# Kernel tuning notes

Hardware: AMD Instinct MI355X
Metric: run time of the kernel (lower is better)

## Reference

```python
import jax, jax.numpy as jnp
import numpy as np

B, G, M, N, RBF, H = 8, 1024, 8, 2048, 50, 128
CUT_LO, CUT_HI = 0.0, 5.0
F = RBF * M * M  # 3200 = in_features of the basis projections


def setup_inputs() -> dict:
    key = jax.random.key(0)
    ks = jax.random.split(key, 8)
    x = jax.random.normal(ks[0], (B, N, 3), dtype=jnp.float32)
    # mapping: linear mixing of fine particles into G groups of M coarse particles
    W_map = jax.random.normal(ks[1], (G, M, N), dtype=jnp.float32) / np.float32(np.sqrt(N))
    W_left = jax.random.normal(ks[2], (H, F), dtype=jnp.float32) / np.float32(np.sqrt(F))
    W_right = jax.random.normal(ks[3], (H, F), dtype=jnp.float32) / np.float32(np.sqrt(F))
    fc1_w = jax.random.normal(ks[4], (H, H), dtype=jnp.float32) / np.float32(np.sqrt(H))
    fc1_b = jax.random.normal(ks[5], (H,), dtype=jnp.float32) * 0.01
    fc2_w = jax.random.normal(ks[6], (1, H), dtype=jnp.float32) / np.float32(np.sqrt(H))
    fc2_b = jax.random.normal(ks[7], (1,), dtype=jnp.float32) * 0.01
    return {"x": x, "W_map": W_map, "W_left": W_left, "W_right": W_right,
            "fc1_w": fc1_w, "fc1_b": fc1_b, "fc2_w": fc2_w, "fc2_b": fc2_b}


def reference(x, W_map, W_left, W_right, fc1_w, fc1_b, fc2_w, fc2_b):
    # ExpNormalSmearing constants (torchmd-net defaults, non-trainable)
    alpha = np.float32(5.0 / (CUT_HI - CUT_LO))
    means = jnp.linspace(np.float32(np.exp(-CUT_HI + CUT_LO)), 1.0, RBF, dtype=jnp.float32)
    beta = np.float32((2.0 / RBF * (1.0 - np.exp(-CUT_HI + CUT_LO))) ** -2)

    # mapping: [B,N,3] -> coarse grained [B,G,M,3]
    xc = jnp.einsum('gmn,bnd->bgmd', W_map, x)
    # pairwise deltas within each group: [B,G,M,M,3]
    delta = xc[:, :, None, :, :] - xc[:, :, :, None, :]
    dn = jnp.sqrt(jnp.sum(delta ** 2, axis=-1, keepdims=True) + 1e-5)  # [B,G,M,M,1]
    # cosine cutoff * exp-normal RBF -> [B,G,M,M,RBF]
    cutoff = 0.5 * (jnp.cos(dn * jnp.pi / CUT_HI) + 1.0) * (dn < CUT_HI)
    sm = cutoff * jnp.exp(-beta * (jnp.exp(alpha * (CUT_LO - dn)) - means) ** 2)
    sm = sm / (dn + 1e-5) ** 2
    # outer-product basis: [B,G,M,M,RBF,3] -> [B,G,F,3]
    basis = (delta[..., None, :] * sm[..., None]).reshape(B, G, F, 3)
    # dual projections over the F axis (Linear applied on swapped axes)
    left = jnp.einsum('hf,bgfd->bghd', W_left, basis)   # [B,G,H,3]
    right = jnp.einsum('hf,bgfd->bghd', W_right, basis)  # [B,G,H,3]
    att = jnp.sum(left * right, axis=-1) + 1e-5          # [B,G,H]
    att = jax.nn.logsumexp(att, axis=-2)                  # pool over groups -> [B,H]
    h = jax.nn.silu(att @ fc1_w.T + fc1_b)
    return h @ fc2_w.T + fc2_b  # [B,1]
```

## Files before the change

kernel.cpp:

```cpp
#include <hip/hip_runtime.h>
#include <hip/hip_bf16.h>
#include <math.h>

#define B_   8
#define G_   1024
#define M_   8
#define N_   2048
#define RBF_ 50
#define H_   128
#define PP_  28
#define RPP  64
#define KSTEPS (PP_*RPP/32)
#define TPB  32

#define OFF_A    0
#define SZ_A     (KSTEPS*16*64*8/2)
#define OFF_XC   (OFF_A + SZ_A)
#define SZ_XC    (B_*G_*M_*3)
#define OFF_ATT  (OFF_XC + SZ_XC)
#define SZ_ATT   (B_*H_*G_)
#define OFF_PART (OFF_ATT + SZ_ATT)
#define SZ_PART  (B_*32*H_*2)

#define M0_   0.006737946999085467f
#define STEP_ 0.020270858224508f
#define BETA_ 633.5087862829640f
#define C2_   25.68448448181152f
#define C3_   0.26031300425529f
#define BC_   0.59416621404589f

typedef __attribute__((ext_vector_type(8))) short s8v;
typedef __attribute__((ext_vector_type(4))) float f4v;

#define LBAR() do { \
    asm volatile("s_waitcnt lgkmcnt(0)\n\ts_barrier" ::: "memory"); \
    __builtin_amdgcn_sched_barrier(0); \
} while (0)

__device__ const int c_pi[28] = {0,0,0,0,0,0,0,1,1,1,1,1,1,2,2,2,2,2,3,3,3,3,4,4,4,5,5,6};
__device__ const int c_pj[28] = {1,2,3,4,5,6,7,2,3,4,5,6,7,3,4,5,6,7,4,5,6,7,5,6,7,6,7,7};

__device__ __forceinline__ unsigned short f2bf(float f) {
    unsigned int b = __float_as_uint(f);
    return (unsigned short)((b + 0x7FFFu + ((b >> 16) & 1u)) >> 16);
}

__global__ __launch_bounds__(256) void k_folda(const float* __restrict__ Wl,
                                               const float* __restrict__ Wr,
                                               float* __restrict__ ws) {
    int t = blockIdx.x * 256 + threadIdx.x;
    int lane = t & 63;
    int mt = (t >> 6) & 15;
    int kstep = t >> 10;
    int pp = kstep >> 1;
    int row = mt * 16 + (lane & 15);
    int side = row >> 7, h = row & 127;
    int r0 = (kstep & 1) * 32 + (lane >> 4) * 8;
    int i = c_pi[pp], j = c_pj[pp];
    const float* src = side ? Wr : Wl;
    const float* pij = src + h * 3200 + (i * 8 + j) * 50;
    const float* pji = src + h * 3200 + (j * 8 + i) * 50;
    s8v v;
#pragma unroll
    for (int e = 0; e < 8; ++e) {
        int r = r0 + e;
        float f = (r < 50) ? (pij[r] - pji[r]) : 0.f;
        v[e] = (short)f2bf(f);
    }
    ((s8v*)(ws + OFF_A))[t] = v;
}

__global__ __launch_bounds__(256, 2) void k_xc(const float* __restrict__ x,
                                               const float* __restrict__ Wm,
                                               float* __restrict__ ws) {
    __shared__ float4 x_s[6][256];
    __shared__ float  red[4][24][68];
    float* xc = ws + OFF_XC;

    int tid = threadIdx.x;
    int wave = tid >> 6, lane = tid & 63;
    int rowbase = blockIdx.x * 16 + wave * 4;

    f4v acc[4][6];
#pragma unroll
    for (int r = 0; r < 4; ++r)
#pragma unroll
        for (int p = 0; p < 6; ++p) acc[r][p] = (f4v)0.f;

#pragma unroll
    for (int p = 0; p < 6; ++p) {
        int bd0 = p * 4;
        float4 v;
        v.x = x[(bd0/3)*6144     + tid*3 + (bd0%3)];
        v.y = x[((bd0+1)/3)*6144 + tid*3 + ((bd0+1)%3)];
        v.z = x[((bd0+2)/3)*6144 + tid*3 + ((bd0+2)%3)];
        v.w = x[((bd0+3)/3)*6144 + tid*3 + ((bd0+3)%3)];
        x_s[p][tid] = v;
    }
    LBAR();

#pragma unroll 1
    for (int nc = 0; nc < 8; ++nc) {
        int n0 = nc * 256;
        float4 pf[6];
        if (nc < 7) {
            int n1 = n0 + 256;
#pragma unroll
            for (int p = 0; p < 6; ++p) {
                int bd0 = p * 4;
                pf[p].x = x[(bd0/3)*6144     + (n1+tid)*3 + (bd0%3)];
                pf[p].y = x[((bd0+1)/3)*6144 + (n1+tid)*3 + ((bd0+1)%3)];
                pf[p].z = x[((bd0+2)/3)*6144 + (n1+tid)*3 + ((bd0+2)%3)];
                pf[p].w = x[((bd0+3)/3)*6144 + (n1+tid)*3 + ((bd0+3)%3)];
            }
        }
        float wv[4][4];
#pragma unroll
        for (int r = 0; r < 4; ++r) {
            const float* wrow = Wm + (size_t)(rowbase + r) * 2048 + n0 + lane;
#pragma unroll
            for (int k = 0; k < 4; ++k) wv[r][k] = wrow[k * 64];
        }
#pragma unroll
        for (int k = 0; k < 4; ++k) {
            int nn = k * 64 + lane;
#pragma unroll
            for (int p = 0; p < 6; ++p) {
                float4 xq = x_s[p][nn];
#pragma unroll
                for (int r = 0; r < 4; ++r) {
                    acc[r][p].x += wv[r][k] * xq.x;
                    acc[r][p].y += wv[r][k] * xq.y;
                    acc[r][p].z += wv[r][k] * xq.z;
                    acc[r][p].w += wv[r][k] * xq.w;
                }
            }
        }
        LBAR();
        if (nc < 7) {
#pragma unroll
            for (int p = 0; p < 6; ++p) x_s[p][tid] = pf[p];
        }
        LBAR();
    }

    int cc = lane;
#pragma unroll 1
    for (int r = 0; r < 4; ++r) {
#pragma unroll
        for (int p = 0; p < 6; ++p) {
            red[wave][p*4+0][lane] = acc[r][p].x;
            red[wave][p*4+1][lane] = acc[r][p].y;
            red[wave][p*4+2][lane] = acc[r][p].z;
            red[wave][p*4+3][lane] = acc[r][p].w;
        }
        if (cc < 24) {
            float s = 0.f;
#pragma unroll
            for (int k = 0; k < 16; ++k) {
                float4 v = *(const float4*)&red[wave][cc][k*4];
                s += (v.x + v.y) + (v.z + v.w);
            }
            int row = rowbase + r;
            int b = cc / 3, d = cc - b * 3;
            xc[(size_t)b*24576 + row*3 + d] = s;
        }
    }
}

__global__ __launch_bounds__(512, 1) void k_main(float* __restrict__ ws) {
    __shared__ __align__(16) char smem[128 * 97 * 4];
    s8v*   Bf = (s8v*)smem;
    float* P  = (float*)smem;

    const float* xc = ws + OFF_XC;
    const s8v* A8 = (const s8v*)(ws + OFF_A);
    float* att = ws + OFF_ATT;

    int tid = threadIdx.x;
    int wave = tid >> 6, lane = tid & 63;
    int p0 = blockIdx.x * TPB;

    int pairL = tid >> 4;
    int sub = tid & 15;
    int rblk = sub >> 2;
    int dsel = sub & 3;
    int pairG = p0 + pairL;
    int bb = pairG >> 10, gg = pairG & 1023;
    const float* xp = xc + ((size_t)bb * 8192 + gg * 8) * 3;

    f4v acc[2][6];
#pragma unroll
    for (int mi = 0; mi < 2; ++mi)
#pragma unroll
        for (int nt = 0; nt < 6; ++nt) acc[mi][nt] = (f4v)0.f;

#pragma unroll 1
    for (int pp = 0; pp < 28; ++pp) {
        s8v afr[2][2];
#pragma unroll
        for (int ksl = 0; ksl < 2; ++ksl) {
            afr[ksl][0] = A8[((pp*2 + ksl)*16 + wave    )*64 + lane];
            afr[ksl][1] = A8[((pp*2 + ksl)*16 + wave + 8)*64 + lane];
        }

        if (dsel < 3) {
            int i = c_pi[pp], j = c_pj[pp];
            float dx = xp[j*3+0] - xp[i*3+0];
            float dy = xp[j*3+1] - xp[i*3+1];
            float dz = xp[j*3+2] - xp[i*3+2];
            float dn = sqrtf(dx*dx + dy*dy + dz*dz + 1e-5f);
            float pref = 0.f;
            if (dn < 5.0f) pref = 0.5f * (cosf(dn * 0.62831853071795865f) + 1.0f);
            float dinv = dn + 1e-5f;
            pref /= (dinv * dinv);
            float ex = expf(-dn);
            int r0 = rblk * 16;
            float d0 = ex - (M0_ + (float)r0 * STEP_);
            float sm    = pref * expf(-BETA_ * d0 * d0);
            float ratio = expf(C2_ * d0 - C3_);
            float smv[16];
#pragma unroll
            for (int q = 0; q < 16; ++q) { smv[q] = sm; sm *= ratio; ratio *= BC_; }
            float dd = (dsel == 0) ? dx : (dsel == 1) ? dy : dz;
            int col = pairL * 3 + dsel;
            int nt = col >> 4, cl = col & 15;
#pragma unroll
            for (int half = 0; half < 2; ++half) {
                int rb = r0 + half * 8;
                int ks = rb >> 5;
                int lf = (((rb >> 3) & 3) << 4) | cl;
                s8v v;
#pragma unroll
                for (int e = 0; e < 8; ++e)
                    v[e] = (short)f2bf(smv[half*8 + e] * dd);
                Bf[(ks*6 + nt)*64 + lf] = v;
            }
        }
        LBAR();

#pragma unroll
        for (int ksl = 0; ksl < 2; ++ksl)
#pragma unroll
            for (int nt = 0; nt < 6; ++nt) {
                s8v bfr = Bf[(ksl*6 + nt)*64 + lane];
#pragma unroll
                for (int mi = 0; mi < 2; ++mi)
                    acc[mi][nt] = __builtin_amdgcn_mfma_f32_16x16x32_bf16(
                        afr[ksl][mi], bfr, acc[mi][nt], 0, 0, 0);
            }
        LBAR();
    }

#pragma unroll
    for (int nt = 0; nt < 6; ++nt)
#pragma unroll
        for (int reg = 0; reg < 4; ++reg) {
            int row = wave*16 + (lane >> 4)*4 + reg;
            int col = nt*16 + (lane & 15);
            P[row*97 + col] = acc[0][nt][reg];
        }
#pragma unroll
    for (int nt = 0; nt < 6; ++nt)
#pragma unroll
        for (int reg = 0; reg < 4; ++reg) {
            int row = wave*16 + (lane >> 4)*4 + reg;
            int col = nt*16 + (lane & 15);
            P[row*97 + col] *= acc[1][nt][reg];
        }
    __syncthreads();
    int h = tid & 127;
    int pr0 = (tid >> 7) * 8;
#pragma unroll
    for (int q = 0; q < 8; ++q) {
        int pr = pr0 + q;
        float a = P[h*97 + pr*3] + P[h*97 + pr*3 + 1] + P[h*97 + pr*3 + 2] + 1e-5f;
        att[(size_t)(p0 + pr) * 128 + h] = a;
    }
}

__global__ __launch_bounds__(256) void k_lse(float* __restrict__ ws) {
    const float* att = ws + OFF_ATT;
    float* part = ws + OFF_PART;
    int blk = blockIdx.x;
    int b = blk >> 5, gblk = blk & 31;
    int tid = threadIdx.x;
    int h = tid & 127, gh = tid >> 7;
    const float* p = att + ((size_t)(b*1024 + gblk*32 + gh*16))*128 + h;
    float m = -1e30f, s = 0.f;
#pragma unroll
    for (int q = 0; q < 16; ++q) {
        float v = p[(size_t)q * 128];
        float nm = fmaxf(m, v);
        s = s * expf(m - nm) + expf(v - nm);
        m = nm;
    }
    __shared__ float mm[256], ss[256];
    mm[tid] = m; ss[tid] = s;
    __syncthreads();
    if (gh == 0) {
        float m2 = mm[tid + 128], s2 = ss[tid + 128];
        float Mv = fmaxf(m, m2);
        float Sv = s * expf(m - Mv) + s2 * expf(m2 - Mv);
        *(float2*)&part[((size_t)(b*32 + gblk)*128 + h)*2] = make_float2(Mv, Sv);
    }
}

__global__ __launch_bounds__(128) void k_mlp(const float* __restrict__ ws,
                                             const float* __restrict__ f1w,
                                             const float* __restrict__ f1b,
                                             const float* __restrict__ f2w,
                                             const float* __restrict__ f2b,
                                             float* __restrict__ out) {
    const float* part = ws + OFF_PART;
    int b = blockIdx.x, h = threadIdx.x;
    float Mv = -1e30f, Sv = 0.f;
#pragma unroll
    for (int k = 0; k < 32; ++k) {
        float2 v = *(const float2*)&part[((size_t)(b*32 + k)*128 + h)*2];
        float nm = fmaxf(Mv, v.x);
        Sv = Sv * expf(Mv - nm) + v.y * expf(v.x - nm);
        Mv = nm;
    }
    float lse = Mv + logf(Sv);
    __shared__ float ls[128];
    ls[h] = lse;
    __syncthreads();
    float acc = f1b[h];
    for (int k = 0; k < 128; ++k) acc += f1w[h*128 + k] * ls[k];
    float v = acc / (1.f + expf(-acc));
    __shared__ float red[128];
    red[h] = v * f2w[h];
    __syncthreads();
    for (int st = 64; st > 0; st >>= 1) {
        if (h < st) red[h] += red[h + st];
        __syncthreads();
    }
    if (h == 0) out[b] = red[0] + f2b[0];
}

extern "C" void kernel_launch(void* const* d_in, const int* in_sizes, int n_in,
                              void* d_out, int out_size, void* d_ws, size_t ws_size,
                              hipStream_t stream) {
    const float* x   = (const float*)d_in[0];
    const float* Wm  = (const float*)d_in[1];
    const float* Wl  = (const float*)d_in[2];
    const float* Wr  = (const float*)d_in[3];
    const float* f1w = (const float*)d_in[4];
    const float* f1b = (const float*)d_in[5];
    const float* f2w = (const float*)d_in[6];
    const float* f2b = (const float*)d_in[7];
    float* ws  = (float*)d_ws;
    float* out = (float*)d_out;

    k_folda<<<224, 256, 0, stream>>>(Wl, Wr, ws);
    k_xc   <<<512, 256, 0, stream>>>(x, Wm, ws);
    k_main <<<256, 512, 0, stream>>>(ws);
    k_lse  <<<256, 256, 0, stream>>>(ws);
    k_mlp  <<<8,   128, 0, stream>>>(ws, f1w, f1b, f2w, f2b, out);
}
```

Before: 224.1 us.

## Retile coarse-graining GEMM with split-K atomics and double-buffer main MFMA loop

Adds a transpose kernel that writes x as [24][N], and rewrites k_xc as a tiled 64-row by 64-k shared-memory GEMM. The K dimension is split four ways across blocks, with register-prefetched double buffers and an atomicAdd reduction into a memset-zeroed xc. In k_main, each group's coordinates are held in registers, the pair loop is fully unrolled with compile-time indices, and the A fragments are prefetched one step ahead. The B tile is double-buffered, which removes one barrier per iteration. The costs are an extra memset and transpose launch, atomic contention, and float results that depend on summation order.

```diff
diff --git a/kernel.cpp b/kernel.cpp
--- a/kernel.cpp
+++ b/kernel.cpp
@@ -21,6 +21,8 @@
 #define SZ_ATT   (B_*H_*G_)
 #define OFF_PART (OFF_ATT + SZ_ATT)
 #define SZ_PART  (B_*32*H_*2)
+#define OFF_XT   (OFF_PART + SZ_PART)
+#define SZ_XT    (24*N_)
 
 #define M0_   0.006737946999085467f
 #define STEP_ 0.020270858224508f
@@ -43,6 +45,14 @@
 __device__ __forceinline__ unsigned short f2bf(float f) {
     unsigned int b = __float_as_uint(f);
     return (unsigned short)((b + 0x7FFFu + ((b >> 16) & 1u)) >> 16);
+}
+
+__global__ __launch_bounds__(256) void k_xt(const float* __restrict__ x,
+                                            float* __restrict__ ws) {
+    int idx = blockIdx.x * 256 + threadIdx.x;
+    int c = idx >> 11, n = idx & 2047;
+    int b = c / 3, d = c - b * 3;
+    ws[OFF_XT + idx] = x[b * 6144 + n * 3 + d];
 }
 
 __global__ __launch_bounds__(256) void k_folda(const float* __restrict__ Wl,
@@ -70,105 +80,96 @@
     ((s8v*)(ws + OFF_A))[t] = v;
 }
 
-__global__ __launch_bounds__(256, 2) void k_xc(const float* __restrict__ x,
-                                               const float* __restrict__ Wm,
+__global__ __launch_bounds__(256, 4) void k_xc(const float* __restrict__ Wm,
                                                float* __restrict__ ws) {
-    __shared__ float4 x_s[6][256];
-    __shared__ float  red[4][24][68];
+    __shared__ __align__(16) float W_s[2][64][65];
+    __shared__ __align__(16) float x_s[2][64][28];
+    const float* xT = ws + OFF_XT;
     float* xc = ws + OFF_XC;
 
     int tid = threadIdx.x;
-    int wave = tid >> 6, lane = tid & 63;
-    int rowbase = blockIdx.x * 16 + wave * 4;
-
-    f4v acc[4][6];
-#pragma unroll
-    for (int r = 0; r < 4; ++r)
-#pragma unroll
-        for (int p = 0; p < 6; ++p) acc[r][p] = (f4v)0.f;
-
-#pragma unroll
-    for (int p = 0; p < 6; ++p) {
-        int bd0 = p * 4;
-        float4 v;
-        v.x = x[(bd0/3)*6144     + tid*3 + (bd0%3)];
-        v.y = x[((bd0+1)/3)*6144 + tid*3 + ((bd0+1)%3)];
-        v.z = x[((bd0+2)/3)*6144 + tid*3 + ((bd0+2)%3)];
-        v.w = x[((bd0+3)/3)*6144 + tid*3 + ((bd0+3)%3)];
-        x_s[p][tid] = v;
-    }
+    int lane = tid & 63, wq = tid >> 6;
+    int rowbase = (blockIdx.x >> 2) * 64;
+    int ks = blockIdx.x & 3;
+    int kb0 = ks * 512;
+
+    int srow = tid >> 4, sk4 = tid & 15;
+    int skk = tid & 63, scs = tid >> 6;
+
+    float acc[24];
+#pragma unroll
+    for (int c = 0; c < 24; ++c) acc[c] = 0.f;
+
+#pragma unroll
+    for (int i = 0; i < 4; ++i)
+        *(float4*)&W_s[0][i*16 + srow][sk4*4] =
+            *(const float4*)&Wm[(size_t)(rowbase + i*16 + srow)*2048 + kb0 + sk4*4];
+#pragma unroll
+    for (int q = 0; q < 6; ++q)
+        x_s[0][skk][scs*6 + q] = xT[(scs*6 + q)*2048 + kb0 + skk];
     LBAR();
 
 #pragma unroll 1
     for (int nc = 0; nc < 8; ++nc) {
-        int n0 = nc * 256;
-        float4 pf[6];
+        int cur = nc & 1;
+        float4 wpf[4];
+        float xpf[6];
         if (nc < 7) {
-            int n1 = n0 + 256;
-#pragma unroll
-            for (int p = 0; p < 6; ++p) {
-                int bd0 = p * 4;
-                pf[p].x = x[(bd0/3)*6144     + (n1+tid)*3 + (bd0%3)];
-                pf[p].y = x[((bd0+1)/3)*6144 + (n1+tid)*3 + ((bd0+1)%3)];
-                pf[p].z = x[((bd0+2)/3)*6144 + (n1+tid)*3 + ((bd0+2)%3)];
-                pf[p].w = x[((bd0+3)/3)*6144 + (n1+tid)*3 + ((bd0+3)%3)];
-            }
-        }
-        float wv[4][4];
-#pragma unroll
-        for (int r = 0; r < 4; ++r) {
-            const float* wrow = Wm + (size_t)(rowbase + r) * 2048 + n0 + lane;
-#pragma unroll
-            for (int k = 0; k < 4; ++k) wv[r][k] = wrow[k * 64];
-        }
-#pragma unroll
-        for (int k = 0; k < 4; ++k) {
-            int nn = k * 64 + lane;
-#pragma unroll
-            for (int p = 0; p < 6; ++p) {
-                float4 xq = x_s[p][nn];
-#pragma unroll
-                for (int r = 0; r < 4; ++r) {
-                    acc[r][p].x += wv[r][k] * xq.x;
-                    acc[r][p].y += wv[r][k] * xq.y;
-                    acc[r][p].z += wv[r][k] * xq.z;
-                    acc[r][p].w += wv[r][k] * xq.w;
-                }
-            }
-        }
-        LBAR();
+            int kb = kb0 + (nc + 1) * 64;
+#pragma unroll
+            for (int i = 0; i < 4; ++i)
+                wpf[i] = *(const float4*)&Wm[(size_t)(rowbase + i*16 + srow)*2048 + kb + sk4*4];
+#pragma unroll
+            for (int q = 0; q < 6; ++q)
+                xpf[q] = xT[(scs*6 + q)*2048 + kb + skk];
+        }
+#pragma unroll
+        for (int k = 0; k < 16; ++k) {
+            int kk = wq * 16 + k;
+            float w = W_s[cur][lane][kk];
+            float4 xv0 = *(const float4*)&x_s[cur][kk][0];
+            float4 xv1 = *(const float4*)&x_s[cur][kk][4];
+            float4 xv2 = *(const float4*)&x_s[cur][kk][8];
+            float4 xv3 = *(const float4*)&x_s[cur][kk][12];
+            float4 xv4 = *(const float4*)&x_s[cur][kk][16];
+            float4 xv5 = *(const float4*)&x_s[cur][kk][20];
+            acc[0]  += w*xv0.x; acc[1]  += w*xv0.y; acc[2]  += w*xv0.z; acc[3]  += w*xv0.w;
+            acc[4]  += w*xv1.x; acc[5]  += w*xv1.y; acc[6]  += w*xv1.z; acc[7]  += w*xv1.w;
+            acc[8]  += w*xv2.x; acc[9]  += w*xv2.y; acc[10] += w*xv2.z; acc[11] += w*xv2.w;
+            acc[12] += w*xv3.x; acc[13] += w*xv3.y; acc[14] += w*xv3.z; acc[15] += w*xv3.w;
+            acc[16] += w*xv4.x; acc[17] += w*xv4.y; acc[18] += w*xv4.z; acc[19] += w*xv4.w;
+            acc[20] += w*xv5.x; acc[21] += w*xv5.y; acc[22] += w*xv5.z; acc[23] += w*xv5.w;
+        }
         if (nc < 7) {
-#pragma unroll
-            for (int p = 0; p < 6; ++p) x_s[p][tid] = pf[p];
-        }
-        LBAR();
-    }
-
-    int cc = lane;
-#pragma unroll 1
-    for (int r = 0; r < 4; ++r) {
-#pragma unroll
-        for (int p = 0; p < 6; ++p) {
-            red[wave][p*4+0][lane] = acc[r][p].x;
-            red[wave][p*4+1][lane] = acc[r][p].y;
-            red[wave][p*4+2][lane] = acc[r][p].z;
-            red[wave][p*4+3][lane] = acc[r][p].w;
-        }
-        if (cc < 24) {
-            float s = 0.f;
-#pragma unroll
-            for (int k = 0; k < 16; ++k) {
-                float4 v = *(const float4*)&red[wave][cc][k*4];
-                s += (v.x + v.y) + (v.z + v.w);
-            }
-            int row = rowbase + r;
-            int b = cc / 3, d = cc - b * 3;
-            xc[(size_t)b*24576 + row*3 + d] = s;
-        }
-    }
-}
-
-__global__ __launch_bounds__(512, 1) void k_main(float* __restrict__ ws) {
+            int nxt = cur ^ 1;
+#pragma unroll
+            for (int i = 0; i < 4; ++i)
+                *(float4*)&W_s[nxt][i*16 + srow][sk4*4] = wpf[i];
+#pragma unroll
+            for (int q = 0; q < 6; ++q)
+                x_s[nxt][skk][scs*6 + q] = xpf[q];
+            LBAR();
+        }
+    }
+
+    LBAR();
+    float* red = &W_s[0][0][0];
+#pragma unroll
+    for (int c = 0; c < 24; ++c)
+        red[(wq*64 + lane)*25 + c] = acc[c];
+    LBAR();
+    int row = tid & 63, c6 = tid >> 6;
+#pragma unroll
+    for (int q = 0; q < 6; ++q) {
+        int c = c6 * 6 + q;
+        float s = red[(0*64 + row)*25 + c] + red[(1*64 + row)*25 + c]
+                + red[(2*64 + row)*25 + c] + red[(3*64 + row)*25 + c];
+        int b = c / 3, d = c - b * 3;
+        atomicAdd(&xc[(size_t)b*24576 + (rowbase + row)*3 + d], s);
+    }
+}
+
+__global__ __launch_bounds__(512, 2) void k_main(float* __restrict__ ws) {
     __shared__ __align__(16) char smem[128 * 97 * 4];
     s8v*   Bf = (s8v*)smem;
     float* P  = (float*)smem;
@@ -176,6 +177,9 @@
     const float* xc = ws + OFF_XC;
     const s8v* A8 = (const s8v*)(ws + OFF_A);
     float* att = ws + OFF_ATT;
+
+    constexpr int pi[28] = {0,0,0,0,0,0,0,1,1,1,1,1,1,2,2,2,2,2,3,3,3,3,4,4,4,5,5,6};
+    constexpr int pj[28] = {1,2,3,4,5,6,7,2,3,4,5,6,7,3,4,5,6,7,4,5,6,7,5,6,7,6,7,7};
 
     int tid = threadIdx.x;
     int wave = tid >> 6, lane = tid & 63;
@@ -186,8 +190,16 @@
     int rblk = sub >> 2;
     int dsel = sub & 3;
     int pairG = p0 + pairL;
-    int bb = pairG >> 10, gg = pairG & 1023;
-    const float* xp = xc + ((size_t)bb * 8192 + gg * 8) * 3;
+
+    float pts[24];
+    {
+        const float4* xq = (const float4*)(xc + (size_t)pairG * 24);
+#pragma unroll
+        for (int q = 0; q < 6; ++q) {
+            float4 v = xq[q];
+            pts[q*4+0] = v.x; pts[q*4+1] = v.y; pts[q*4+2] = v.z; pts[q*4+3] = v.w;
+        }
+    }
 
     f4v acc[2][6];
 #pragma unroll
@@ -195,28 +207,27 @@
 #pragma unroll
         for (int nt = 0; nt < 6; ++nt) acc[mi][nt] = (f4v)0.f;
 
-#pragma unroll 1
+    s8v afr[2][2], afn[2][2];
+#pragma unroll
+    for (int ksl = 0; ksl < 2; ++ksl) {
+        afr[ksl][0] = A8[((0*2 + ksl)*16 + wave    )*64 + lane];
+        afr[ksl][1] = A8[((0*2 + ksl)*16 + wave + 8)*64 + lane];
+    }
+
+#pragma unroll
     for (int pp = 0; pp < 28; ++pp) {
-        s8v afr[2][2];
-#pragma unroll
-        for (int ksl = 0; ksl < 2; ++ksl) {
-            afr[ksl][0] = A8[((pp*2 + ksl)*16 + wave    )*64 + lane];
-            afr[ksl][1] = A8[((pp*2 + ksl)*16 + wave + 8)*64 + lane];
-        }
-
+        s8v* Bq = Bf + (pp & 1) * 768;
         if (dsel < 3) {
-            int i = c_pi[pp], j = c_pj[pp];
-            float dx = xp[j*3+0] - xp[i*3+0];
-            float dy = xp[j*3+1] - xp[i*3+1];
-            float dz = xp[j*3+2] - xp[i*3+2];
+            float dx = pts[pj[pp]*3+0] - pts[pi[pp]*3+0];
+            float dy = pts[pj[pp]*3+1] - pts[pi[pp]*3+1];
+            float dz = pts[pj[pp]*3+2] - pts[pi[pp]*3+2];
             float dn = sqrtf(dx*dx + dy*dy + dz*dz + 1e-5f);
             float pref = 0.f;
             if (dn < 5.0f) pref = 0.5f * (cosf(dn * 0.62831853071795865f) + 1.0f);
             float dinv = dn + 1e-5f;
             pref /= (dinv * dinv);
             float ex = expf(-dn);
-            int r0 = rblk * 16;
-            float d0 = ex - (M0_ + (float)r0 * STEP_);
+            float d0 = ex - (M0_ + (float)(rblk*16) * STEP_);
             float sm    = pref * expf(-BETA_ * d0 * d0);
             float ratio = expf(C2_ * d0 - C3_);
             float smv[16];
@@ -227,31 +238,42 @@
             int nt = col >> 4, cl = col & 15;
 #pragma unroll
             for (int half = 0; half < 2; ++half) {
-                int rb = r0 + half * 8;
-                int ks = rb >> 5;
+                int rb = rblk*16 + half * 8;
+                int ksw = rb >> 5;
                 int lf = (((rb >> 3) & 3) << 4) | cl;
                 s8v v;
 #pragma unroll
                 for (int e = 0; e < 8; ++e)
                     v[e] = (short)f2bf(smv[half*8 + e] * dd);
-                Bf[(ks*6 + nt)*64 + lf] = v;
+                Bq[(ksw*6 + nt)*64 + lf] = v;
             }
         }
+        if (pp < 27) {
+#pragma unroll
+            for (int ksl = 0; ksl < 2; ++ksl) {
+                afn[ksl][0] = A8[(((pp+1)*2 + ksl)*16 + wave    )*64 + lane];
+                afn[ksl][1] = A8[(((pp+1)*2 + ksl)*16 + wave + 8)*64 + lane];
+            }
+        }
         LBAR();
-
 #pragma unroll
         for (int ksl = 0; ksl < 2; ++ksl)
 #pragma unroll
             for (int nt = 0; nt < 6; ++nt) {
-                s8v bfr = Bf[(ksl*6 + nt)*64 + lane];
+                s8v bfr = Bq[(ksl*6 + nt)*64 + lane];
 #pragma unroll
                 for (int mi = 0; mi < 2; ++mi)
                     acc[mi][nt] = __builtin_amdgcn_mfma_f32_16x16x32_bf16(
                         afr[ksl][mi], bfr, acc[mi][nt], 0, 0, 0);
             }
-        LBAR();
-    }
-
+#pragma unroll
+        for (int ksl = 0; ksl < 2; ++ksl) {
+            afr[ksl][0] = afn[ksl][0];
+            afr[ksl][1] = afn[ksl][1];
+        }
+    }
+
+    LBAR();
 #pragma unroll
     for (int nt = 0; nt < 6; ++nt)
 #pragma unroll
@@ -353,8 +375,10 @@
     float* ws  = (float*)d_ws;
     float* out = (float*)d_out;
 
+    hipMemsetAsync(ws + OFF_XC, 0, SZ_XC * sizeof(float), stream);
+    k_xt   <<<192, 256, 0, stream>>>(x, ws);
     k_folda<<<224, 256, 0, stream>>>(Wl, Wr, ws);
-    k_xc   <<<512, 256, 0, stream>>>(x, Wm, ws);
+    k_xc   <<<512, 256, 0, stream>>>(Wm, ws);
     k_main <<<256, 512, 0, stream>>>(ws);
     k_lse  <<<256, 256, 0, stream>>>(ws);
     k_mlp  <<<8,   128, 0, stream>>>(ws, f1w, f1b, f2w, f2b, out);
```

Measured after the change: 208.5 us. 6.9% less time.
